# Kernel tuning notes

Hardware: AMD Instinct MI355X
Metric: run time of the kernel (lower is better)

## Reference

```python
import jax, jax.numpy as jnp
import numpy as np

H, C = 5, 12            # heads, head_size
N_NODES, N_EDGES = 100000, 1600000
F_NODE, F_EDGE = 128, 32
HID, N_CLASSES = 16, 2


def _lin_init(key, din, dout, bias=True):
    k1, k2 = jax.random.split(key)
    s = 1.0 / np.sqrt(din)
    W = jax.random.uniform(k1, (din, dout), minval=-s, maxval=s, dtype=jnp.float32)
    if bias:
        b = jax.random.uniform(k2, (dout,), minval=-s, maxval=s, dtype=jnp.float32)
        return W, b
    return W


def setup_inputs() -> dict:
    key = jax.random.key(0)
    ks = jax.random.split(key, 8)
    d = {}
    d["x"] = jax.random.normal(ks[0], (N_NODES, F_NODE), dtype=jnp.float32)
    d["edge_index"] = jax.random.randint(ks[1], (2, N_EDGES), 0, N_NODES)
    d["edge_attr"] = jax.random.normal(ks[2], (N_EDGES, F_EDGE), dtype=jnp.float32)
    HC = H * C
    for i, din in [(1, F_NODE), (2, HC)]:
        kk = jax.random.split(ks[2 + i], 5)
        d[f"Wq{i}"], d[f"bq{i}"] = _lin_init(kk[0], din, HC)
        d[f"Wk{i}"], d[f"bk{i}"] = _lin_init(kk[1], din, HC)
        d[f"Wv{i}"], d[f"bv{i}"] = _lin_init(kk[2], din, HC)
        d[f"We{i}"] = _lin_init(kk[3], F_EDGE, HC, bias=False)  # lin_edge has no bias in PyG
        d[f"Ws{i}"], d[f"bs{i}"] = _lin_init(kk[4], din, HC)    # root/skip linear
    d["W1"], d["b1"] = _lin_init(ks[6], HC, HID)
    d["W2"], d["b2"] = _lin_init(ks[7], HID, N_CLASSES)
    return d


def _transformer_conv(x, src, dst, edge_attr, Wq, bq, Wk, bk, Wv, bv, We, Ws, bs):
    # PyG TransformerConv, concat=True, root_weight=True, beta=False, dropout=0
    N = x.shape[0]
    q = (x @ Wq + bq).reshape(N, H, C)
    k = (x @ Wk + bk).reshape(N, H, C)
    v = (x @ Wv + bv).reshape(N, H, C)
    e = (edge_attr @ We).reshape(-1, H, C)          # [E,H,C]
    kj = k[src] + e                                  # per-edge key
    vj = v[src] + e                                  # per-edge value
    alpha = jnp.einsum('ehc,ehc->eh', q[dst], kj) / jnp.sqrt(jnp.asarray(C, x.dtype))
    # segment-softmax over incoming edges of each destination node
    amax = jax.ops.segment_max(alpha, dst, num_segments=N)          # [N,H]
    w = jnp.exp(alpha - amax[dst])
    denom = jax.ops.segment_sum(w, dst, num_segments=N)             # [N,H]
    w = w / (denom[dst] + 1e-16)
    out = jax.ops.segment_sum(vj * w[:, :, None], dst, num_segments=N).reshape(N, H * C)
    return out + x @ Ws + bs                                         # skip/root connection


def reference(x, edge_index, edge_attr,
              Wq1, bq1, Wk1, bk1, Wv1, bv1, We1, Ws1, bs1,
              Wq2, bq2, Wk2, bk2, Wv2, bv2, We2, Ws2, bs2,
              W1, b1, W2, b2):
    src, dst = edge_index[0], edge_index[1]
    h = jax.nn.relu(_transformer_conv(x, src, dst, edge_attr, Wq1, bq1, Wk1, bk1, Wv1, bv1, We1, Ws1, bs1))
    h = jax.nn.relu(_transformer_conv(h, src, dst, edge_attr, Wq2, bq2, Wk2, bk2, Wv2, bv2, We2, Ws2, bs2))
    h = jax.nn.relu(h @ W1 + b1)
    return h @ W2 + b2
```

## Files before the change

kernel.cpp:

```cpp
#include <hip/hip_runtime.h>
#include <cstddef>

#define NN 100000
#define NE 1600000
#define NH 5
#define NC 12
#define HC 60
#define FN 128
#define FE 32
#define HID 16
#define NCLS 2

typedef float v4f __attribute__((ext_vector_type(4)));
typedef _Float16 h2 __attribute__((ext_vector_type(2)));
typedef _Float16 h8 __attribute__((ext_vector_type(8)));

#if __has_builtin(__builtin_amdgcn_exp2f)
#define EXP2F(x) __builtin_amdgcn_exp2f(x)
#else
#define EXP2F(x) exp2f(x)
#endif

__device__ __forceinline__ float bperm(int idxb, float x) {
    return __int_as_float(__builtin_amdgcn_ds_bpermute(idxb, __float_as_int(x)));
}

__device__ __forceinline__ float dot2h(unsigned int u, h2 w, float c) {
    const h2 a = __builtin_bit_cast(h2, u);
#if __has_builtin(__builtin_amdgcn_fdot2)
    return __builtin_amdgcn_fdot2(a, w, c, false);
#else
    return fmaf((float)a[0], (float)w[0], fmaf((float)a[1], (float)w[1], c));
#endif
}

template<int DIN>
__global__ __launch_bounds__(256) void qkvs_kernel(
    const float* __restrict__ X,
    const float* __restrict__ Wq, const float* __restrict__ bq,
    const float* __restrict__ Wk, const float* __restrict__ bk,
    const float* __restrict__ Wv, const float* __restrict__ bv,
    const float* __restrict__ Ws, const float* __restrict__ bs,
    float* __restrict__ qb, float* __restrict__ kvb, float* __restrict__ sb)
{
    constexpr int NB = 16;
    __shared__ float xs[NB][DIN + 5];
    const int n0 = blockIdx.x * NB;
    for (int i = threadIdx.x; i < NB * DIN; i += 256) {
        const int nd = i / DIN, r = i - nd * DIN;
        xs[nd][r] = X[(size_t)(n0 + nd) * DIN + r];
    }
    __syncthreads();

    const int t = threadIdx.x;
    if (t >= 240) return;
    const int cg = t % 60, ng = t / 60;
    const int mat = cg / 15, q4 = (cg % 15) * 4;
    const float* W; const float* b; float* outp; int ostr;
    switch (mat) {
        case 0:  W = Wq; b = bq; outp = qb;       ostr = 60;  break;
        case 1:  W = Wk; b = bk; outp = kvb;      ostr = 120; break;
        case 2:  W = Wv; b = bv; outp = kvb + 60; ostr = 120; break;
        default: W = Ws; b = bs; outp = sb;       ostr = 60;  break;
    }
    float acc[4][4] = {};
    #pragma unroll 2
    for (int r = 0; r < DIN; ++r) {
        const float4 w = *(const float4*)(W + r * 60 + q4);
        #pragma unroll
        for (int j = 0; j < 4; ++j) {
            const float xv = xs[4 * ng + j][r];
            acc[j][0] = fmaf(xv, w.x, acc[j][0]);
            acc[j][1] = fmaf(xv, w.y, acc[j][1]);
            acc[j][2] = fmaf(xv, w.z, acc[j][2]);
            acc[j][3] = fmaf(xv, w.w, acc[j][3]);
        }
    }
    const float4 bb = *(const float4*)(b + q4);
    #pragma unroll
    for (int j = 0; j < 4; ++j) {
        float4 o;
        o.x = acc[j][0] + bb.x; o.y = acc[j][1] + bb.y;
        o.z = acc[j][2] + bb.z; o.w = acc[j][3] + bb.w;
        *(float4*)(outp + (size_t)(n0 + 4 * ng + j) * ostr + q4) = o;
    }
}

__global__ __launch_bounds__(256) void hist_kernel(
    const int* __restrict__ ei, int* __restrict__ cnt)
{
    const int e = blockIdx.x * 256 + threadIdx.x;
    if (e < NE) atomicAdd(&cnt[ei[NE + e]], 1);
}

__global__ __launch_bounds__(1024) void scan1_kernel(
    const int* __restrict__ cnt, int* __restrict__ excl, int* __restrict__ bsum)
{
    __shared__ int sh[1024];
    const int i = blockIdx.x * 1024 + threadIdx.x;
    const int v = (i < NN) ? cnt[i] : 0;
    sh[threadIdx.x] = v;
    __syncthreads();
    for (int off = 1; off < 1024; off <<= 1) {
        const int t = (threadIdx.x >= off) ? sh[threadIdx.x - off] : 0;
        __syncthreads();
        sh[threadIdx.x] += t;
        __syncthreads();
    }
    if (i < NN) excl[i] = sh[threadIdx.x] - v;
    if (threadIdx.x == 1023) bsum[blockIdx.x] = sh[1023];
}

__global__ __launch_bounds__(128) void scan2_kernel(
    int* __restrict__ bsum, int nb, int* __restrict__ start)
{
    __shared__ int sh[128];
    const int i = threadIdx.x;
    const int v = (i < nb) ? bsum[i] : 0;
    sh[i] = v;
    __syncthreads();
    for (int off = 1; off < 128; off <<= 1) {
        const int tv = (i >= off) ? sh[i - off] : 0;
        __syncthreads();
        sh[i] += tv;
        __syncthreads();
    }
    if (i < nb) bsum[i] = sh[i] - v;
    if (i == 127) start[NN] = sh[127];
}

__global__ __launch_bounds__(1024) void scan3_kernel(
    int* __restrict__ start, const int* __restrict__ bsum)
{
    const int i = blockIdx.x * 1024 + threadIdx.x;
    if (i < NN) start[i] += bsum[blockIdx.x];
}

__global__ __launch_bounds__(256) void scatter_kernel(
    const int* __restrict__ ei, int* __restrict__ cursor,
    int* __restrict__ perm, int* __restrict__ srcs)
{
    const int e = blockIdx.x * 256 + threadIdx.x;
    if (e >= NE) return;
    const int d = ei[NE + e];
    const int pos = atomicAdd(&cursor[d], 1);
    perm[pos] = e;
    srcs[pos] = ei[e];
}

__global__ __launch_bounds__(256) void permea_kernel(
    const int* __restrict__ perm, const float* __restrict__ ea,
    h8* __restrict__ eaPh)
{
    const int t = blockIdx.x * 256 + threadIdx.x;
    const int slot = t >> 2, part = t & 3;
    const int e = perm[slot];
    const float4* src = (const float4*)(ea + (size_t)e * FE) + 2 * part;
    const float4 a = src[0];
    const float4 b = src[1];
    h8 o;
    o[0] = (_Float16)a.x; o[1] = (_Float16)a.y;
    o[2] = (_Float16)a.z; o[3] = (_Float16)a.w;
    o[4] = (_Float16)b.x; o[5] = (_Float16)b.y;
    o[6] = (_Float16)b.z; o[7] = (_Float16)b.w;
    eaPh[(size_t)slot * 4 + part] = o;
}

template<bool LIN>
__global__ __launch_bounds__(256) void agg_kernel(
    const int* __restrict__ perm, const int* __restrict__ srcs,
    const int* __restrict__ start,
    const _Float16* __restrict__ eaH, const float* __restrict__ eaF,
    const float* __restrict__ We,
    const float* __restrict__ q, const float* __restrict__ kv,
    const float* __restrict__ sk, float* __restrict__ hout)
{
    const int wv    = threadIdx.x >> 6;
    const int lane  = threadIdx.x & 63;
    const int n     = blockIdx.x * 4 + wv;
    const int hc    = (lane < 60) ? lane : 0;
    const int hd    = hc / NC;
    const int hbase = hd * NC;
    const int c     = hc - hbase;

    const int i1 = (hbase + (c + 3) % 12) << 2;
    const int i2 = (hbase + (c + 6) % 12) << 2;
    const int i3 = (hbase + (c + 9) % 12) << 2;
    const int j1 = (hbase + (c + 1) % 3) << 2;
    const int j2 = (hbase + (c + 2) % 3) << 2;

    const float qv = q[(size_t)n * 60 + hc];
    const float sv = sk[(size_t)n * 60 + hc];

    const int s0 = __builtin_amdgcn_readfirstlane(start[n]);
    const int s1 = __builtin_amdgcn_readfirstlane(start[n + 1]);

    float acc = 0.f, den = 0.f;

    auto tail = [&](float eacc, float KV, float VV) {
        const float p = qv * (KV + eacc);
        const float f = (p + bperm(i1, p)) + (bperm(i2, p) + bperm(i3, p));
        const float a = (f + bperm(j1, f)) + bperm(j2, f);
        const float w = EXP2F(fmaf(a, 0.41647013f, -28.8539009f));
        acc = fmaf(w, VV + eacc, acc);
        den += w;
    };

    if constexpr (LIN) {
        h2 WH[16];
        #pragma unroll
        for (int p = 0; p < 16; ++p) {
            h2 w;
            w[0] = (_Float16)We[(2 * p)     * 60 + hc];
            w[1] = (_Float16)We[(2 * p + 1) * 60 + hc];
            WH[p] = w;
        }

        auto load_ea = [&](uint4 (&E)[4], int tt) {
            const uint4* er = (const uint4*)(eaH + (size_t)tt * FE);
            #pragma unroll
            for (int i = 0; i < 4; ++i) E[i] = er[i];
        };
        auto compute = [&](const uint4 (&E)[4], float KV, float VV) {
            float d0 = 0.f, d1 = 0.f;
            #pragma unroll
            for (int i = 0; i < 4; ++i) {
                d0 = dot2h(E[i].x, WH[4 * i + 0], d0);
                d1 = dot2h(E[i].y, WH[4 * i + 1], d1);
                d0 = dot2h(E[i].z, WH[4 * i + 2], d0);
                d1 = dot2h(E[i].w, WH[4 * i + 3], d1);
            }
            tail(d0 + d1, KV, VV);
        };

        uint4 eaA[4], eaB[4];
        float kA = 0.f, vA = 0.f, kB = 0.f, vB = 0.f;
        float kC = 0.f, vC = 0.f, kD = 0.f, vD = 0.f;

        if (s0 < s1) {
            {
                const int sa = srcs[s0];
                kA = kv[(size_t)sa * 120 + hc];
                vA = kv[(size_t)sa * 120 + 60 + hc];
                if (s0 + 1 < s1) {
                    const int sb_ = srcs[s0 + 1];
                    kB = kv[(size_t)sb_ * 120 + hc];
                    vB = kv[(size_t)sb_ * 120 + 60 + hc];
                }
                load_ea(eaA, s0);
            }
            for (int t = s0; t < s1; t += 2) {
                if (t + 1 < s1) load_ea(eaB, t + 1);
                if (t + 2 < s1) {
                    const int sc_ = srcs[t + 2];
                    kC = kv[(size_t)sc_ * 120 + hc];
                    vC = kv[(size_t)sc_ * 120 + 60 + hc];
                }
                compute(eaA, kA, vA);
                if (t + 2 < s1) load_ea(eaA, t + 2);
                if (t + 3 < s1) {
                    const int sd_ = srcs[t + 3];
                    kD = kv[(size_t)sd_ * 120 + hc];
                    vD = kv[(size_t)sd_ * 120 + 60 + hc];
                }
                if (t + 1 < s1) compute(eaB, kB, vB);
                kA = kC; vA = vC; kB = kD; vB = vD;
            }
        }
    } else {
        float Wcol[FE];
        #pragma unroll
        for (int r = 0; r < FE; ++r) Wcol[r] = We[r * 60 + hc];
        for (int t = s0; t < s1; ++t) {
            const int e = perm[t];
            const float* __restrict__ er = eaF + (size_t)e * FE;
            float e0 = 0.f, e1 = 0.f;
            #pragma unroll
            for (int r = 0; r < FE; r += 2) {
                e0 = fmaf(er[r],     Wcol[r],     e0);
                e1 = fmaf(er[r + 1], Wcol[r + 1], e1);
            }
            const int sa = srcs[t];
            const float KV = kv[(size_t)sa * 120 + hc];
            const float VV = kv[(size_t)sa * 120 + 60 + hc];
            tail(e0 + e1, KV, VV);
        }
    }

    if (lane < 60)
        hout[(size_t)n * 60 + hc] = fmaxf(acc / (den + 1e-16f) + sv, 0.f);
}

__global__ __launch_bounds__(256) void mlp_kernel(
    const float* __restrict__ h,
    const float* __restrict__ W1, const float* __restrict__ b1,
    const float* __restrict__ W2, const float* __restrict__ b2,
    float* __restrict__ out)
{
    __shared__ float sW1[60 * HID];
    __shared__ float sb1[HID];
    __shared__ float sW2[HID * NCLS];
    __shared__ float sb2[NCLS];
    for (int i = threadIdx.x; i < 60 * HID; i += 256) sW1[i] = W1[i];
    if (threadIdx.x < HID)        sb1[threadIdx.x] = b1[threadIdx.x];
    if (threadIdx.x < HID * NCLS) sW2[threadIdx.x] = W2[threadIdx.x];
    if (threadIdx.x < NCLS)       sb2[threadIdx.x] = b2[threadIdx.x];
    __syncthreads();

    const int n = blockIdx.x * 256 + threadIdx.x;
    if (n >= NN) return;
    const float* __restrict__ hr = h + (size_t)n * 60;
    float hv[60];
    #pragma unroll
    for (int i = 0; i < 15; ++i) {
        const float4 t = ((const float4*)hr)[i];
        hv[4 * i + 0] = t.x; hv[4 * i + 1] = t.y;
        hv[4 * i + 2] = t.z; hv[4 * i + 3] = t.w;
    }
    float o0 = sb2[0], o1 = sb2[1];
    for (int j = 0; j < HID; ++j) {
        float t = sb1[j];
        #pragma unroll
        for (int i = 0; i < 60; ++i) t = fmaf(hv[i], sW1[i * HID + j], t);
        t = fmaxf(t, 0.f);
        o0 = fmaf(t, sW2[2 * j + 0], o0);
        o1 = fmaf(t, sW2[2 * j + 1], o1);
    }
    out[(size_t)n * 2 + 0] = o0;
    out[(size_t)n * 2 + 1] = o1;
}

extern "C" void kernel_launch(void* const* d_in, const int* in_sizes, int n_in,
                              void* d_out, int out_size, void* d_ws, size_t ws_size,
                              hipStream_t stream)
{
    const float* x   = (const float*)d_in[0];
    const int*   ei  = (const int*)  d_in[1];
    const float* ea  = (const float*)d_in[2];
    const float* Wq1 = (const float*)d_in[3];  const float* bq1 = (const float*)d_in[4];
    const float* Wk1 = (const float*)d_in[5];  const float* bk1 = (const float*)d_in[6];
    const float* Wv1 = (const float*)d_in[7];  const float* bv1 = (const float*)d_in[8];
    const float* We1 = (const float*)d_in[9];
    const float* Ws1 = (const float*)d_in[10]; const float* bs1 = (const float*)d_in[11];
    const float* Wq2 = (const float*)d_in[12]; const float* bq2 = (const float*)d_in[13];
    const float* Wk2 = (const float*)d_in[14]; const float* bk2 = (const float*)d_in[15];
    const float* Wv2 = (const float*)d_in[16]; const float* bv2 = (const float*)d_in[17];
    const float* We2 = (const float*)d_in[18];
    const float* Ws2 = (const float*)d_in[19]; const float* bs2 = (const float*)d_in[20];
    const float* W1  = (const float*)d_in[21]; const float* b1  = (const float*)d_in[22];
    const float* W2  = (const float*)d_in[23]; const float* b2  = (const float*)d_in[24];
    float* out = (float*)d_out;

    int* cnt    = (int*)d_ws;
    int* startp = cnt + NN;
    int* cursor = startp + NN + 1;
    int* bsum   = cursor + NN;
    int* perm   = bsum + 128;
    int* srcs   = perm + NE;
    const size_t int_bytes = (size_t)(3 * NN + 1 + 128 + 2 * NE) * sizeof(int);
    const size_t f_off = (int_bytes + 255) & ~(size_t)255;
    const size_t NHC = (size_t)NN * 60;
    float* qb  = (float*)((char*)d_ws + f_off);
    float* kvb = qb + NHC;
    float* sb  = kvb + 2 * NHC;
    float* h0  = sb + NHC;
    _Float16* eaPh = (_Float16*)(h0 + NHC);
    const size_t need = f_off + 5 * NHC * sizeof(float)
                      + (size_t)NE * FE * sizeof(_Float16);
    const bool lin = ws_size >= need;

    const int qkvs_blocks = NN / 16;
    const int e256_blocks = NE / 256;
    const int scan_blocks = (NN + 1023) / 1024;
    const int agg_blocks  = NN / 4;
    const int mlp_blocks  = (NN + 255) / 256;
    const int perm_blocks = NE * 4 / 256;

    hipMemsetAsync(cnt, 0, (size_t)NN * sizeof(int), stream);
    hist_kernel<<<e256_blocks, 256, 0, stream>>>(ei, cnt);
    scan1_kernel<<<scan_blocks, 1024, 0, stream>>>(cnt, startp, bsum);
    scan2_kernel<<<1, 128, 0, stream>>>(bsum, scan_blocks, startp);
    scan3_kernel<<<scan_blocks, 1024, 0, stream>>>(startp, bsum);
    hipMemcpyAsync(cursor, startp, (size_t)NN * sizeof(int),
                   hipMemcpyDeviceToDevice, stream);
    scatter_kernel<<<e256_blocks, 256, 0, stream>>>(ei, cursor, perm, srcs);
    if (lin)
        permea_kernel<<<perm_blocks, 256, 0, stream>>>(perm, ea, (h8*)eaPh);

    qkvs_kernel<FN><<<qkvs_blocks, 256, 0, stream>>>(
        x, Wq1, bq1, Wk1, bk1, Wv1, bv1, Ws1, bs1, qb, kvb, sb);
    if (lin)
        agg_kernel<true><<<agg_blocks, 256, 0, stream>>>(
            perm, srcs, startp, eaPh, ea, We1, qb, kvb, sb, h0);
    else
        agg_kernel<false><<<agg_blocks, 256, 0, stream>>>(
            perm, srcs, startp, eaPh, ea, We1, qb, kvb, sb, h0);

    qkvs_kernel<HC><<<qkvs_blocks, 256, 0, stream>>>(
        h0, Wq2, bq2, Wk2, bk2, Wv2, bv2, Ws2, bs2, qb, kvb, sb);
    if (lin)
        agg_kernel<true><<<agg_blocks, 256, 0, stream>>>(
            perm, srcs, startp, eaPh, ea, We2, qb, kvb, sb, h0);
    else
        agg_kernel<false><<<agg_blocks, 256, 0, stream>>>(
            perm, srcs, startp, eaPh, ea, We2, qb, kvb, sb, h0);

    mlp_kernel<<<mlp_blocks, 256, 0, stream>>>(h0, W1, b1, W2, b2, out);
}
```

Baseline: 1.184 ms.

## Interleave two nodes per wave in aggregation, rework QKVS GEMM, fuse cursor copy

The aggregation kernel now has each wave process two destination nodes, n and n+NN/2, with their edge loops interleaved. The intent is more independent loads in flight per wave to hide gather latency, at the cost of more registers and divergence when the two degrees differ. The QKVS projection kernel drops the shared-memory staging of X. Each wave now computes one weight matrix for 16 nodes, reading X rows directly with packed two-wide FMAs. The separate device-to-device cursor memcpy is also folded into scan3, which writes the cursor array directly.

```diff
diff --git a/kernel.cpp b/kernel.cpp
--- a/kernel.cpp
+++ b/kernel.cpp
@@ -12,6 +12,7 @@
 #define NCLS 2
 
 typedef float v4f __attribute__((ext_vector_type(4)));
+typedef float f2v __attribute__((ext_vector_type(2)));
 typedef _Float16 h2 __attribute__((ext_vector_type(2)));
 typedef _Float16 h8 __attribute__((ext_vector_type(8)));
 
@@ -31,6 +32,18 @@
     return __builtin_amdgcn_fdot2(a, w, c, false);
 #else
     return fmaf((float)a[0], (float)w[0], fmaf((float)a[1], (float)w[1], c));
+#endif
+}
+
+__device__ __forceinline__ f2v mk2(float a, float b) {
+    f2v t; t[0] = a; t[1] = b; return t;
+}
+__device__ __forceinline__ f2v fma2(f2v a, float w, f2v c) {
+#if __has_builtin(__builtin_elementwise_fma)
+    f2v ww; ww[0] = w; ww[1] = w;
+    return __builtin_elementwise_fma(a, ww, c);
+#else
+    f2v r; r[0] = fmaf(a[0], w, c[0]); r[1] = fmaf(a[1], w, c[1]); return r;
 #endif
 }
 
@@ -44,45 +57,40 @@
     float* __restrict__ qb, float* __restrict__ kvb, float* __restrict__ sb)
 {
     constexpr int NB = 16;
-    __shared__ float xs[NB][DIN + 5];
     const int n0 = blockIdx.x * NB;
-    for (int i = threadIdx.x; i < NB * DIN; i += 256) {
-        const int nd = i / DIN, r = i - nd * DIN;
-        xs[nd][r] = X[(size_t)(n0 + nd) * DIN + r];
-    }
-    __syncthreads();
-
-    const int t = threadIdx.x;
-    if (t >= 240) return;
-    const int cg = t % 60, ng = t / 60;
-    const int mat = cg / 15, q4 = (cg % 15) * 4;
+    const int w = threadIdx.x >> 6, lane = threadIdx.x & 63;
+    const int cl = (lane < 60) ? lane : 0;
     const float* W; const float* b; float* outp; int ostr;
-    switch (mat) {
+    switch (w) {
         case 0:  W = Wq; b = bq; outp = qb;       ostr = 60;  break;
         case 1:  W = Wk; b = bk; outp = kvb;      ostr = 120; break;
         case 2:  W = Wv; b = bv; outp = kvb + 60; ostr = 120; break;
         default: W = Ws; b = bs; outp = sb;       ostr = 60;  break;
     }
-    float acc[4][4] = {};
-    #pragma unroll 2
-    for (int r = 0; r < DIN; ++r) {
-        const float4 w = *(const float4*)(W + r * 60 + q4);
+    const float* __restrict__ xr = X + (size_t)n0 * DIN;
+    f2v acc[8] = {};
+    for (int r = 0; r < DIN; r += 4) {
+        const float w0 = W[(r + 0) * 60 + cl];
+        const float w1 = W[(r + 1) * 60 + cl];
+        const float w2 = W[(r + 2) * 60 + cl];
+        const float w3 = W[(r + 3) * 60 + cl];
         #pragma unroll
-        for (int j = 0; j < 4; ++j) {
-            const float xv = xs[4 * ng + j][r];
-            acc[j][0] = fmaf(xv, w.x, acc[j][0]);
-            acc[j][1] = fmaf(xv, w.y, acc[j][1]);
-            acc[j][2] = fmaf(xv, w.z, acc[j][2]);
-            acc[j][3] = fmaf(xv, w.w, acc[j][3]);
-        }
-    }
-    const float4 bb = *(const float4*)(b + q4);
-    #pragma unroll
-    for (int j = 0; j < 4; ++j) {
-        float4 o;
-        o.x = acc[j][0] + bb.x; o.y = acc[j][1] + bb.y;
-        o.z = acc[j][2] + bb.z; o.w = acc[j][3] + bb.w;
-        *(float4*)(outp + (size_t)(n0 + 4 * ng + j) * ostr + q4) = o;
+        for (int p = 0; p < 8; ++p) {
+            const float4 xa = *(const float4*)(xr + (size_t)(2 * p)     * DIN + r);
+            const float4 xb = *(const float4*)(xr + (size_t)(2 * p + 1) * DIN + r);
+            acc[p] = fma2(mk2(xa.x, xb.x), w0, acc[p]);
+            acc[p] = fma2(mk2(xa.y, xb.y), w1, acc[p]);
+            acc[p] = fma2(mk2(xa.z, xb.z), w2, acc[p]);
+            acc[p] = fma2(mk2(xa.w, xb.w), w3, acc[p]);
+        }
+    }
+    if (lane < 60) {
+        const float bb = b[lane];
+        #pragma unroll
+        for (int p = 0; p < 8; ++p) {
+            outp[(size_t)(n0 + 2 * p)     * ostr + lane] = acc[p][0] + bb;
+            outp[(size_t)(n0 + 2 * p + 1) * ostr + lane] = acc[p][1] + bb;
+        }
     }
 }
 
@@ -130,10 +138,15 @@
 }
 
 __global__ __launch_bounds__(1024) void scan3_kernel(
-    int* __restrict__ start, const int* __restrict__ bsum)
+    int* __restrict__ start, const int* __restrict__ bsum,
+    int* __restrict__ cursor)
 {
     const int i = blockIdx.x * 1024 + threadIdx.x;
-    if (i < NN) start[i] += bsum[blockIdx.x];
+    if (i < NN) {
+        const int v = start[i] + bsum[blockIdx.x];
+        start[i] = v;
+        cursor[i] = v;
+    }
 }
 
 __global__ __launch_bounds__(256) void scatter_kernel(
@@ -175,10 +188,9 @@
     const float* __restrict__ q, const float* __restrict__ kv,
     const float* __restrict__ sk, float* __restrict__ hout)
 {
-    const int wv    = threadIdx.x >> 6;
-    const int lane  = threadIdx.x & 63;
-    const int n     = blockIdx.x * 4 + wv;
-    const int hc    = (lane < 60) ? lane : 0;
+    const int wv   = threadIdx.x >> 6;
+    const int lane = threadIdx.x & 63;
+    const int hc   = (lane < 60) ? lane : 0;
     const int hd    = hc / NC;
     const int hbase = hd * NC;
     const int c     = hc - hbase;
@@ -189,39 +201,44 @@
     const int j1 = (hbase + (c + 1) % 3) << 2;
     const int j2 = (hbase + (c + 2) % 3) << 2;
 
-    const float qv = q[(size_t)n * 60 + hc];
-    const float sv = sk[(size_t)n * 60 + hc];
-
-    const int s0 = __builtin_amdgcn_readfirstlane(start[n]);
-    const int s1 = __builtin_amdgcn_readfirstlane(start[n + 1]);
-
-    float acc = 0.f, den = 0.f;
-
-    auto tail = [&](float eacc, float KV, float VV) {
+    auto tail = [&](float eacc, float KV, float VV, float qv,
+                    float& A, float& D) {
         const float p = qv * (KV + eacc);
         const float f = (p + bperm(i1, p)) + (bperm(i2, p) + bperm(i3, p));
         const float a = (f + bperm(j1, f)) + bperm(j2, f);
         const float w = EXP2F(fmaf(a, 0.41647013f, -28.8539009f));
-        acc = fmaf(w, VV + eacc, acc);
-        den += w;
+        A = fmaf(w, VV + eacc, A);
+        D += w;
     };
 
     if constexpr (LIN) {
+        const int g  = blockIdx.x * 4 + wv;
+        const int n1 = g, n2 = g + NN / 2;
+
         h2 WH[16];
         #pragma unroll
         for (int p = 0; p < 16; ++p) {
-            h2 w;
-            w[0] = (_Float16)We[(2 * p)     * 60 + hc];
-            w[1] = (_Float16)We[(2 * p + 1) * 60 + hc];
-            WH[p] = w;
-        }
-
-        auto load_ea = [&](uint4 (&E)[4], int tt) {
-            const uint4* er = (const uint4*)(eaH + (size_t)tt * FE);
-            #pragma unroll
-            for (int i = 0; i < 4; ++i) E[i] = er[i];
-        };
-        auto compute = [&](const uint4 (&E)[4], float KV, float VV) {
+            h2 wvv;
+            wvv[0] = (_Float16)We[(2 * p)     * 60 + hc];
+            wvv[1] = (_Float16)We[(2 * p + 1) * 60 + hc];
+            WH[p] = wvv;
+        }
+
+        const float qv1 = q[(size_t)n1 * 60 + hc];
+        const float sv1 = sk[(size_t)n1 * 60 + hc];
+        const float qv2 = q[(size_t)n2 * 60 + hc];
+        const float sv2 = sk[(size_t)n2 * 60 + hc];
+
+        const int a0 = __builtin_amdgcn_readfirstlane(start[n1]);
+        const int a1 = __builtin_amdgcn_readfirstlane(start[n1 + 1]);
+        const int b0 = __builtin_amdgcn_readfirstlane(start[n2]);
+        const int b1 = __builtin_amdgcn_readfirstlane(start[n2 + 1]);
+        const int c1 = a1 - a0, c2 = b1 - b0;
+        const int mx = (c1 > c2) ? c1 : c2;
+
+        float acc1 = 0.f, den1 = 0.f, acc2 = 0.f, den2 = 0.f;
+
+        auto drow = [&](const uint4 (&E)[4]) -> float {
             float d0 = 0.f, d1 = 0.f;
             #pragma unroll
             for (int i = 0; i < 4; ++i) {
@@ -230,65 +247,70 @@
                 d0 = dot2h(E[i].z, WH[4 * i + 2], d0);
                 d1 = dot2h(E[i].w, WH[4 * i + 3], d1);
             }
-            tail(d0 + d1, KV, VV);
+            return d0 + d1;
         };
-
-        uint4 eaA[4], eaB[4];
-        float kA = 0.f, vA = 0.f, kB = 0.f, vB = 0.f;
-        float kC = 0.f, vC = 0.f, kD = 0.f, vD = 0.f;
-
-        if (s0 < s1) {
-            {
-                const int sa = srcs[s0];
-                kA = kv[(size_t)sa * 120 + hc];
-                vA = kv[(size_t)sa * 120 + 60 + hc];
-                if (s0 + 1 < s1) {
-                    const int sb_ = srcs[s0 + 1];
-                    kB = kv[(size_t)sb_ * 120 + hc];
-                    vB = kv[(size_t)sb_ * 120 + 60 + hc];
-                }
-                load_ea(eaA, s0);
-            }
-            for (int t = s0; t < s1; t += 2) {
-                if (t + 1 < s1) load_ea(eaB, t + 1);
-                if (t + 2 < s1) {
-                    const int sc_ = srcs[t + 2];
-                    kC = kv[(size_t)sc_ * 120 + hc];
-                    vC = kv[(size_t)sc_ * 120 + 60 + hc];
-                }
-                compute(eaA, kA, vA);
-                if (t + 2 < s1) load_ea(eaA, t + 2);
-                if (t + 3 < s1) {
-                    const int sd_ = srcs[t + 3];
-                    kD = kv[(size_t)sd_ * 120 + hc];
-                    vD = kv[(size_t)sd_ * 120 + 60 + hc];
-                }
-                if (t + 1 < s1) compute(eaB, kB, vB);
-                kA = kC; vA = vC; kB = kD; vB = vD;
-            }
+        auto ldea = [&](uint4 (&E)[4], int t) {
+            const uint4* er = (const uint4*)(eaH + (size_t)t * FE);
+            E[0] = er[0]; E[1] = er[1]; E[2] = er[2]; E[3] = er[3];
+        };
+        auto ldkv = [&](float& K, float& V, int t) {
+            const float* r = kv + (size_t)srcs[t] * 120;
+            K = r[hc]; V = r[60 + hc];
+        };
+
+        uint4 eA1[4], eB1[4], eA2[4], eB2[4];
+        float kA1 = 0.f, vA1 = 0.f, kB1 = 0.f, vB1 = 0.f;
+        float kA2 = 0.f, vA2 = 0.f, kB2 = 0.f, vB2 = 0.f;
+
+        if (c1 > 0) { ldkv(kA1, vA1, a0);     ldea(eA1, a0);     }
+        if (c1 > 1) { ldkv(kB1, vB1, a0 + 1); ldea(eB1, a0 + 1); }
+        if (c2 > 0) { ldkv(kA2, vA2, b0);     ldea(eA2, b0);     }
+        if (c2 > 1) { ldkv(kB2, vB2, b0 + 1); ldea(eB2, b0 + 1); }
+
+        for (int i = 0; i < mx; i += 2) {
+            if (i < c1)     tail(drow(eA1), kA1, vA1, qv1, acc1, den1);
+            if (i < c2)     tail(drow(eA2), kA2, vA2, qv2, acc2, den2);
+            if (i + 2 < c1) { ldkv(kA1, vA1, a0 + i + 2); ldea(eA1, a0 + i + 2); }
+            if (i + 2 < c2) { ldkv(kA2, vA2, b0 + i + 2); ldea(eA2, b0 + i + 2); }
+            if (i + 1 < c1) tail(drow(eB1), kB1, vB1, qv1, acc1, den1);
+            if (i + 1 < c2) tail(drow(eB2), kB2, vB2, qv2, acc2, den2);
+            if (i + 3 < c1) { ldkv(kB1, vB1, a0 + i + 3); ldea(eB1, a0 + i + 3); }
+            if (i + 3 < c2) { ldkv(kB2, vB2, b0 + i + 3); ldea(eB2, b0 + i + 3); }
+        }
+
+        if (lane < 60) {
+            hout[(size_t)n1 * 60 + hc] = fmaxf(acc1 / (den1 + 1e-16f) + sv1, 0.f);
+            hout[(size_t)n2 * 60 + hc] = fmaxf(acc2 / (den2 + 1e-16f) + sv2, 0.f);
         }
     } else {
         float Wcol[FE];
         #pragma unroll
         for (int r = 0; r < FE; ++r) Wcol[r] = We[r * 60 + hc];
-        for (int t = s0; t < s1; ++t) {
-            const int e = perm[t];
-            const float* __restrict__ er = eaF + (size_t)e * FE;
-            float e0 = 0.f, e1 = 0.f;
-            #pragma unroll
-            for (int r = 0; r < FE; r += 2) {
-                e0 = fmaf(er[r],     Wcol[r],     e0);
-                e1 = fmaf(er[r + 1], Wcol[r + 1], e1);
+        const int g = blockIdx.x * 4 + wv;
+        #pragma unroll 1
+        for (int pass = 0; pass < 2; ++pass) {
+            const int n = pass ? (g + NN / 2) : g;
+            const float qv = q[(size_t)n * 60 + hc];
+            const float sv = sk[(size_t)n * 60 + hc];
+            const int s0 = __builtin_amdgcn_readfirstlane(start[n]);
+            const int s1 = __builtin_amdgcn_readfirstlane(start[n + 1]);
+            float acc = 0.f, den = 0.f;
+            for (int t = s0; t < s1; ++t) {
+                const int e = perm[t];
+                const float* __restrict__ er = eaF + (size_t)e * FE;
+                float e0 = 0.f, e1 = 0.f;
+                #pragma unroll
+                for (int r = 0; r < FE; r += 2) {
+                    e0 = fmaf(er[r],     Wcol[r],     e0);
+                    e1 = fmaf(er[r + 1], Wcol[r + 1], e1);
+                }
+                const float* kr = kv + (size_t)srcs[t] * 120;
+                tail(e0 + e1, kr[hc], kr[60 + hc], qv, acc, den);
             }
-            const int sa = srcs[t];
-            const float KV = kv[(size_t)sa * 120 + hc];
-            const float VV = kv[(size_t)sa * 120 + 60 + hc];
-            tail(e0 + e1, KV, VV);
-        }
-    }
-
-    if (lane < 60)
-        hout[(size_t)n * 60 + hc] = fmaxf(acc / (den + 1e-16f) + sv, 0.f);
+            if (lane < 60)
+                hout[(size_t)n * 60 + hc] = fmaxf(acc / (den + 1e-16f) + sv, 0.f);
+        }
+    }
 }
 
 __global__ __launch_bounds__(256) void mlp_kernel(
@@ -372,7 +394,7 @@
     const int qkvs_blocks = NN / 16;
     const int e256_blocks = NE / 256;
     const int scan_blocks = (NN + 1023) / 1024;
-    const int agg_blocks  = NN / 4;
+    const int agg_blocks  = NN / 8;
     const int mlp_blocks  = (NN + 255) / 256;
     const int perm_blocks = NE * 4 / 256;
 
@@ -380,9 +402,7 @@
     hist_kernel<<<e256_blocks, 256, 0, stream>>>(ei, cnt);
     scan1_kernel<<<scan_blocks, 1024, 0, stream>>>(cnt, startp, bsum);
     scan2_kernel<<<1, 128, 0, stream>>>(bsum, scan_blocks, startp);
-    scan3_kernel<<<scan_blocks, 1024, 0, stream>>>(startp, bsum);
-    hipMemcpyAsync(cursor, startp, (size_t)NN * sizeof(int),
-                   hipMemcpyDeviceToDevice, stream);
+    scan3_kernel<<<scan_blocks, 1024, 0, stream>>>(startp, bsum, cursor);
     scatter_kernel<<<e256_blocks, 256, 0, stream>>>(ei, cursor, perm, srcs);
     if (lin)
         permea_kernel<<<perm_blocks, 256, 0, stream>>>(perm, ea, (h8*)eaPh);
```

New measurement: 1.311 ms. 1.11x slower.
